# Optimization experiments

Measured on AMD Instinct MI355X. Metric: run time of the kernel, lower is better.

The kernel has to match this reference:

```python
import jax, jax.numpy as jnp
import numpy as np

N, E, DIN, H, M, O = 100000, 3200000, 128, 256, 500, 100


def setup_inputs() -> dict:
    key = jax.random.key(0)
    ks = jax.random.split(key, 8)
    x = jax.random.normal(ks[0], (N, DIN), dtype=jnp.float32)
    edge_index = jax.random.randint(ks[1], (2, E), 0, N, dtype=jnp.int64)
    # GCNConv weights (glorot-ish scale) and biases
    W1 = jax.random.normal(ks[2], (DIN, H), dtype=jnp.float32) / np.sqrt(DIN)
    b1 = jnp.zeros((H,), dtype=jnp.float32)
    W2 = jax.random.normal(ks[3], (H, M), dtype=jnp.float32) / np.sqrt(H)
    b2 = jnp.zeros((M,), dtype=jnp.float32)
    # output head ('GO'): Linear(M -> O)
    Wout = jax.random.normal(ks[4], (M, O), dtype=jnp.float32) / np.sqrt(M)
    bout = jnp.zeros((O,), dtype=jnp.float32)
    # threshold param stored as inv_softplus(1.0) so softplus(threshold)=1.0
    threshold = jnp.float32(np.log(np.expm1(1.0)))
    return {"x": x, "edge_index": edge_index, "W1": W1, "b1": b1,
            "W2": W2, "b2": b2, "Wout": Wout, "bout": bout,
            "threshold": threshold}


def reference(x, edge_index, W1, b1, W2, b2, Wout, bout, threshold):
    src, dst = edge_index[0], edge_index[1]
    n = x.shape[0]
    # GCN sym-normalization with improved=True (self-loop weight 2):
    # deg[i] = 2 + #incoming edges; norm(e) = deg^-1/2[src] * deg^-1/2[dst]
    deg = jax.ops.segment_sum(jnp.ones(src.shape[0], x.dtype), dst,
                              num_segments=n) + jnp.asarray(2.0, x.dtype)
    dinv = jax.lax.rsqrt(deg)
    coef = dinv[src] * dinv[dst]              # [E]
    self_coef = (2.0 * dinv * dinv)[:, None]  # [N,1] self-loop term

    def gcn_conv(h, W, b):
        h = h @ W                              # [N,C]
        agg = jax.ops.segment_sum(h[src] * coef[:, None], dst, num_segments=n)
        return agg + self_coef * h + b

    h = jax.nn.relu(gcn_conv(x, W1, b1))       # conv + ReLU (no bn, no dropout)
    module_representation = jax.nn.softplus(gcn_conv(h, W2, b2))  # [N,M]
    # tanh probability transform: tanh(softplus(threshold) * x)
    p = jnp.tanh(jax.nn.softplus(threshold) * module_representation)
    y_go = p @ Wout + bout                     # output head 'GO'
    return (module_representation, y_go)
```

## Files before the change

### kernel.cpp

```cpp
#include <hip/hip_runtime.h>
#include <cstdint>
#include <cstddef>

#define DIN 128
#define HID 256
#define MODD 500
#define OUTD 100

typedef unsigned int uint;
typedef unsigned short ushort;
typedef __attribute__((ext_vector_type(8))) __bf16 bf16x8;
typedef __attribute__((ext_vector_type(4))) float f32x4;

__device__ __forceinline__ float bf2f(ushort u) {
    return __uint_as_float(((uint)u) << 16);
}
__device__ __forceinline__ ushort f2bf(float f) {
    uint u = __float_as_uint(f);
    return (ushort)((u + 0x7FFF + ((u >> 16) & 1)) >> 16);
}
__device__ __forceinline__ uint packbf2(float lo, float hi) {
    return (uint)f2bf(lo) | ((uint)f2bf(hi) << 16);
}
__device__ __forceinline__ void async_copy16(const void* g, void* l) {
    __builtin_amdgcn_global_load_lds((const __attribute__((address_space(1))) void*)g,
                                     (__attribute__((address_space(3))) void*)l, 16, 0, 0);
}
__device__ __forceinline__ float tanh_fast(float x) {
    return 1.0f - 2.0f / (__expf(2.0f * x) + 1.0f);
}
__device__ __forceinline__ float softplus_fast(float v) {
    return fmaxf(v, 0.0f) + __logf(1.0f + __expf(-fabsf(v)));
}
__device__ __forceinline__ void acc8(float* a, uint4 v, float w) {
    a[0] += w * bf2f((ushort)(v.x & 0xFFFF));
    a[1] += w * bf2f((ushort)(v.x >> 16));
    a[2] += w * bf2f((ushort)(v.y & 0xFFFF));
    a[3] += w * bf2f((ushort)(v.y >> 16));
    a[4] += w * bf2f((ushort)(v.z & 0xFFFF));
    a[5] += w * bf2f((ushort)(v.z >> 16));
    a[6] += w * bf2f((ushort)(v.w & 0xFFFF));
    a[7] += w * bf2f((ushort)(v.w >> 16));
}


__global__ void count_deg(const int* __restrict__ dst, int* __restrict__ deg, int E) {
    int e = blockIdx.x * blockDim.x + threadIdx.x;
    if (e < E) atomicAdd(&deg[dst[e]], 1);
}

__global__ void compute_dinv(const int* __restrict__ deg, float* __restrict__ dinv, int N) {
    int i = blockIdx.x * blockDim.x + threadIdx.x;
    if (i < N) dinv[i] = rsqrtf((float)deg[i] + 2.0f);
}

__global__ void scan_block(const int* __restrict__ deg, int* __restrict__ rp,
                           int* __restrict__ bsum, int n) {
    __shared__ int wsum[16];
    int tid = threadIdx.x;
    int lane = tid & 63;
    int w = tid >> 6;
    int i = blockIdx.x * 1024 + tid;
    int v = (i < n) ? deg[i] : 0;
    int x = v;
    #pragma unroll
    for (int off = 1; off < 64; off <<= 1) {
        int t = __shfl_up(x, off);
        if (lane >= off) x += t;
    }
    if (lane == 63) wsum[w] = x;
    __syncthreads();
    if (tid == 0) {
        int s = 0;
        #pragma unroll
        for (int k = 0; k < 16; ++k) { int t = wsum[k]; wsum[k] = s; s += t; }
        bsum[blockIdx.x] = s;
    }
    __syncthreads();
    if (i < n) rp[i] = wsum[w] + (x - v);
}

__global__ void scan_bsums(int* __restrict__ bsum, int nb) {
    if (threadIdx.x == 0 && blockIdx.x == 0) {
        int s = 0;
        for (int k = 0; k < nb; ++k) { int t = bsum[k]; bsum[k] = s; s += t; }
        bsum[nb] = s;
    }
}

__global__ void scan_add(int* __restrict__ rp, const int* __restrict__ bsum, int n, int nb) {
    int i = blockIdx.x * blockDim.x + threadIdx.x;
    if (i < n) rp[i] += bsum[i >> 10];
    else if (i == n) rp[n] = bsum[nb];
}


#define BSH 9
#define MAXB 256
#define PCH 8192

__global__ void init_bucket_cursor(const int* __restrict__ rp, int* __restrict__ bcur,
                                   int NB) {
    int b = blockIdx.x * blockDim.x + threadIdx.x;
    if (b < NB) bcur[b] = rp[b << BSH];
}

__global__ __launch_bounds__(256)
void partition_edges(const int* __restrict__ src, const int* __restrict__ dst,
                     int* __restrict__ bcur, uint* __restrict__ pairBuf,
                     int E, int NB) {
    __shared__ int hist[MAXB];
    __shared__ int gbase[MAXB];
    int tid = threadIdx.x;
    int e0 = blockIdx.x * PCH;
    int e1 = min(e0 + PCH, E);
    for (int b = tid; b < NB; b += 256) hist[b] = 0;
    __syncthreads();
    for (int e = e0 + tid; e < e1; e += 256) {
        int d = dst[e];
        atomicAdd(&hist[d >> BSH], 1);
    }
    __syncthreads();
    for (int b = tid; b < NB; b += 256) {
        int h = hist[b];
        gbase[b] = h ? atomicAdd(&bcur[b], h) : 0;
        hist[b] = 0;
    }
    __syncthreads();
    for (int e = e0 + tid; e < e1; e += 256) {
        int d = dst[e];
        int s = src[e];
        int b = d >> BSH;
        int idx = gbase[b] + atomicAdd(&hist[b], 1);
        pairBuf[idx] = (uint)s | ((uint)(d & ((1 << BSH) - 1)) << 20);
    }
}

__global__ __launch_bounds__(512)
void bucket_scatter(const uint* __restrict__ pairBuf, const int* __restrict__ rp,
                    int* __restrict__ col, int N) {
    __shared__ int lcur[1 << BSH];
    int b = blockIdx.x;
    int n0 = b << BSH;
    int nn = min(1 << BSH, N - n0);
    int tid = threadIdx.x;
    for (int i = tid; i < nn; i += 512) lcur[i] = rp[n0 + i];
    __syncthreads();
    int start = rp[n0];
    int end = rp[min(n0 + (1 << BSH), N)];
    for (int e = start + tid; e < end; e += 512) {
        uint v = pairBuf[e];
        int doff = v >> 20;
        int s = v & 0xFFFFF;
        int pos = atomicAdd(&lcur[doff], 1);
        col[pos] = s;
    }
}


__global__ void cast_f32_bf16(const float* __restrict__ src, ushort* __restrict__ dst, int n4) {
    int i = blockIdx.x * blockDim.x + threadIdx.x;
    if (i < n4) {
        float4 v = ((const float4*)src)[i];
        ushort4 o;
        o.x = f2bf(v.x); o.y = f2bf(v.y); o.z = f2bf(v.z); o.w = f2bf(v.w);
        ((ushort4*)dst)[i] = o;
    }
}

__global__ void transpose_cast(const float* __restrict__ src, ushort* __restrict__ dst,
                               int K, int N, int Kpad, int Npad) {
    int idx = blockIdx.x * blockDim.x + threadIdx.x;
    if (idx >= Npad * Kpad) return;
    int n = idx / Kpad, k = idx - n * Kpad;
    float v = (n < N && k < K) ? src[(size_t)k * N + n] : 0.0f;
    dst[idx] = f2bf(v);
}


__global__ void aggregate128(const ushort* __restrict__ X, ushort* __restrict__ Y,
                             const int* __restrict__ rp, const int* __restrict__ col,
                             const float* __restrict__ dinv, int N) {
    int gw = blockIdx.x * (blockDim.x >> 6) + (threadIdx.x >> 6);
    int lane = threadIdx.x & 63;
    if (gw >= N) return;
    int g = lane >> 4;
    int sub = lane & 15;
    float di = dinv[gw];
    float sc = 2.0f * di * di;
    const uint4* Xr = (const uint4*)X;
    float a[8] = {};
    if (g == 0) acc8(a, Xr[(size_t)gw * 16 + sub], sc);
    int e = rp[gw], end = rp[gw + 1];
    int base = e;
    for (; base + 8 <= end; base += 8) {
        int c0 = col[base + g];
        int c1 = col[base + 4 + g];
        float w0 = dinv[c0] * di, w1 = dinv[c1] * di;
        uint4 v0 = Xr[(size_t)c0 * 16 + sub];
        uint4 v1 = Xr[(size_t)c1 * 16 + sub];
        acc8(a, v0, w0);
        acc8(a, v1, w1);
    }
    if (base + 4 <= end) {
        int c0 = col[base + g];
        float w0 = dinv[c0] * di;
        acc8(a, Xr[(size_t)c0 * 16 + sub], w0);
        base += 4;
    }
    int rem = end - base;
    if (g < rem) {
        int c0 = col[base + g];
        float w0 = dinv[c0] * di;
        acc8(a, Xr[(size_t)c0 * 16 + sub], w0);
    }
    #pragma unroll
    for (int q = 0; q < 8; ++q) {
        a[q] += __shfl_xor(a[q], 16);
        a[q] += __shfl_xor(a[q], 32);
    }
    if (g == 0) {
        uint4 o;
        o.x = packbf2(a[0], a[1]);
        o.y = packbf2(a[2], a[3]);
        o.z = packbf2(a[4], a[5]);
        o.w = packbf2(a[6], a[7]);
        ((uint4*)Y)[(size_t)gw * 16 + sub] = o;
    }
}

__global__ void aggregate256(const ushort* __restrict__ X, ushort* __restrict__ Y,
                             const int* __restrict__ rp, const int* __restrict__ col,
                             const float* __restrict__ dinv, int N) {
    int gw = blockIdx.x * (blockDim.x >> 6) + (threadIdx.x >> 6);
    int lane = threadIdx.x & 63;
    if (gw >= N) return;
    int g = lane >> 5;
    int sub = lane & 31;
    float di = dinv[gw];
    float sc = 2.0f * di * di;
    const uint4* Xr = (const uint4*)X;
    float a[8] = {};
    if (g == 0) acc8(a, Xr[(size_t)gw * 32 + sub], sc);
    int e = rp[gw], end = rp[gw + 1];
    int base = e;
    for (; base + 4 <= end; base += 4) {
        int c0 = col[base + g];
        int c1 = col[base + 2 + g];
        float w0 = dinv[c0] * di, w1 = dinv[c1] * di;
        uint4 v0 = Xr[(size_t)c0 * 32 + sub];
        uint4 v1 = Xr[(size_t)c1 * 32 + sub];
        acc8(a, v0, w0);
        acc8(a, v1, w1);
    }
    if (base + 2 <= end) {
        int c0 = col[base + g];
        float w0 = dinv[c0] * di;
        acc8(a, Xr[(size_t)c0 * 32 + sub], w0);
        base += 2;
    }
    if (base < end && g == 0) {
        int c0 = col[base];
        float w0 = dinv[c0] * di;
        acc8(a, Xr[(size_t)c0 * 32 + sub], w0);
    }
    #pragma unroll
    for (int q = 0; q < 8; ++q) a[q] += __shfl_xor(a[q], 32);
    if (g == 0) {
        uint4 o;
        o.x = packbf2(a[0], a[1]);
        o.y = packbf2(a[2], a[3]);
        o.z = packbf2(a[4], a[5]);
        o.w = packbf2(a[6], a[7]);
        ((uint4*)Y)[(size_t)gw * 32 + sub] = o;
    }
}


template<int K, int MODE>
__global__ __launch_bounds__(256)
void gemm_bt(const ushort* __restrict__ A, const ushort* __restrict__ BT,
             const float* __restrict__ bias, void* __restrict__ Cout,
             int M, int Nact, int ldc, ushort* __restrict__ C2,
             const float* __restrict__ thr) {
    __shared__ ushort sA[128 * 32];
    __shared__ ushort sB[128 * 32];
    int tid = threadIdx.x;
    int lane = tid & 63;
    int w = tid >> 6;
    int wr = w >> 1, wc = w & 1;
    int row0 = blockIdx.y * 128;
    int col0 = blockIdx.x * 128;
    float sp = 0.0f;
    if (MODE == 3) sp = softplus_fast(*thr);
    f32x4 acc[4][4] = {};

    for (int kt = 0; kt < K; kt += 32) {
        if (kt) __syncthreads();
        #pragma unroll
        for (int L = 0; L < 2; ++L) {
            int cb = L * 256 + w * 64;
            int c = cb + lane;
            int r = c >> 2;
            int ko = (c & 3) * 8;
            int rr = min(row0 + r, M - 1);
            async_copy16(A + (size_t)rr * K + kt + ko, sA + (size_t)cb * 8);
        }
        #pragma unroll
        for (int L = 0; L < 2; ++L) {
            int cb = L * 256 + w * 64;
            int c = cb + lane;
            int nr = c >> 2;
            int ko = (c & 3) * 8;
            async_copy16(BT + (size_t)(col0 + nr) * K + kt + ko, sB + (size_t)cb * 8);
        }
        __syncthreads();
        bf16x8 af[4], bfr[4];
        #pragma unroll
        for (int i = 0; i < 4; ++i) {
            int row = wr * 64 + i * 16 + (lane & 15);
            af[i] = *(const bf16x8*)(sA + row * 32 + (lane >> 4) * 8);
        }
        #pragma unroll
        for (int j = 0; j < 4; ++j) {
            int n = wc * 64 + j * 16 + (lane & 15);
            bfr[j] = *(const bf16x8*)(sB + n * 32 + (lane >> 4) * 8);
        }
        #pragma unroll
        for (int i = 0; i < 4; ++i)
            #pragma unroll
            for (int j = 0; j < 4; ++j)
                acc[i][j] = __builtin_amdgcn_mfma_f32_16x16x32_bf16(af[i], bfr[j], acc[i][j], 0, 0, 0);
    }

    #pragma unroll
    for (int i = 0; i < 4; ++i) {
        #pragma unroll
        for (int j = 0; j < 4; ++j) {
            int col = col0 + wc * 64 + j * 16 + (lane & 15);
            if (MODE == 3) {
                bool act = (col < Nact);
                float bv = act ? bias[col] : 0.0f;
                #pragma unroll
                for (int r = 0; r < 4; ++r) {
                    int row = row0 + wr * 64 + i * 16 + (lane >> 4) * 4 + r;
                    if (row >= M) continue;
                    if (act) {
                        float v = softplus_fast(acc[i][j][r] + bv);
                        ((float*)Cout)[(size_t)row * ldc + col] = v;
                        C2[(size_t)row * 512 + col] = f2bf(tanh_fast(sp * v));
                    } else {
                        C2[(size_t)row * 512 + col] = 0;
                    }
                }
            } else {
                if (col >= Nact) continue;
                float bv = bias[col];
                #pragma unroll
                for (int r = 0; r < 4; ++r) {
                    int row = row0 + wr * 64 + i * 16 + (lane >> 4) * 4 + r;
                    if (row >= M) continue;
                    float v = acc[i][j][r] + bv;
                    if (MODE == 0) {
                        v = fmaxf(v, 0.0f);
                        ((ushort*)Cout)[(size_t)row * ldc + col] = f2bf(v);
                    } else {
                        ((float*)Cout)[(size_t)row * ldc + col] = v;
                    }
                }
            }
        }
    }
}


extern "C" void kernel_launch(void* const* d_in, const int* in_sizes, int n_in,
                              void* d_out, int out_size, void* d_ws, size_t ws_size,
                              hipStream_t stream) {
    const float* x    = (const float*)d_in[0];
    const int*   ei   = (const int*)d_in[1];
    const float* W1   = (const float*)d_in[2];
    const float* b1   = (const float*)d_in[3];
    const float* W2   = (const float*)d_in[4];
    const float* b2   = (const float*)d_in[5];
    const float* Wout = (const float*)d_in[6];
    const float* bout = (const float*)d_in[7];
    const float* thr  = (const float*)d_in[8];

    int N = in_sizes[0] / DIN;
    int E = in_sizes[1] / 2;
    const int* srcI = ei;
    const int* dstI = ei + E;

    char* wsp = (char*)d_ws;
    size_t o = 0;
    auto alloc = [&](size_t bytes) -> void* {
        void* p = wsp + o;
        o = (o + bytes + 255) & ~(size_t)255;
        return p;
    };
    int*    deg   = (int*)alloc((size_t)N * 4);
    float*  dinv  = (float*)alloc((size_t)N * 4);
    int*    rp    = (int*)alloc((size_t)(N + 1) * 4);
    int*    bsum  = (int*)alloc(1024);
    int*    bcur  = (int*)alloc(MAXB * 4);
    ushort* W1T   = (ushort*)alloc((size_t)256 * 128 * 2);
    ushort* W2T   = (ushort*)alloc((size_t)512 * 256 * 2);
    ushort* WoutT = (ushort*)alloc((size_t)128 * 512 * 2);
    ushort* bufA  = (ushort*)alloc((size_t)N * 256 * 2);
    size_t  col_off = o;
    int*    col   = (int*)alloc((size_t)E * 4);
    ushort* hbuf  = (ushort*)alloc((size_t)N * 256 * 2);
    size_t  pbf_need = col_off + (size_t)N * 512 * 2;
    if (o < pbf_need) o = (pbf_need + 255) & ~(size_t)255;
    ushort* pbf = (ushort*)(wsp + col_off);

    ushort* xbf = bufA;
    ushort* xa  = bufA + (size_t)N * 128;
    ushort* ha  = bufA;
    uint* pairBuf = (uint*)hbuf;

    float* mr   = (float*)d_out;
    float* yout = (float*)d_out + (size_t)N * MODD;

    int mtiles = (N + 127) / 128;
    int NB = (N + (1 << BSH) - 1) >> BSH;

    hipMemsetAsync(deg, 0, (size_t)N * 4, stream);
    count_deg<<<(E + 255) / 256, 256, 0, stream>>>(dstI, deg, E);
    compute_dinv<<<(N + 255) / 256, 256, 0, stream>>>(deg, dinv, N);
    int nb = (N + 1023) / 1024;
    scan_block<<<nb, 1024, 0, stream>>>(deg, rp, bsum, N);
    scan_bsums<<<1, 64, 0, stream>>>(bsum, nb);
    scan_add<<<(N + 256) / 256, 256, 0, stream>>>(rp, bsum, N, nb);
    init_bucket_cursor<<<1, 256, 0, stream>>>(rp, bcur, NB);
    partition_edges<<<(E + PCH - 1) / PCH, 256, 0, stream>>>(srcI, dstI, bcur, pairBuf, E, NB);
    bucket_scatter<<<NB, 512, 0, stream>>>(pairBuf, rp, col, N);

    cast_f32_bf16<<<((N * DIN / 4) + 255) / 256, 256, 0, stream>>>(x, xbf, N * DIN / 4);
    transpose_cast<<<(256 * 128 + 255) / 256, 256, 0, stream>>>(W1, W1T, 128, 256, 128, 256);
    transpose_cast<<<(512 * 256 + 255) / 256, 256, 0, stream>>>(W2, W2T, 256, 500, 256, 512);
    transpose_cast<<<(128 * 512 + 255) / 256, 256, 0, stream>>>(Wout, WoutT, 500, 100, 512, 128);

    aggregate128<<<(N + 3) / 4, 256, 0, stream>>>(xbf, xa, rp, col, dinv, N);
    gemm_bt<128, 0><<<dim3(2, mtiles), 256, 0, stream>>>(xa, W1T, b1, hbuf, N, HID, HID,
                                                         nullptr, nullptr);

    aggregate256<<<(N + 3) / 4, 256, 0, stream>>>(hbuf, ha, rp, col, dinv, N);
    gemm_bt<256, 3><<<dim3(4, mtiles), 256, 0, stream>>>(ha, W2T, b2, mr, N, MODD, MODD,
                                                         pbf, thr);

    gemm_bt<512, 2><<<dim3(1, mtiles), 256, 0, stream>>>(pbf, WoutT, bout, yout, N, OUTD, OUTD,
                                                         nullptr, nullptr);
}
```

Measured before the change: 1.072 ms.

## Sort edges by source bin within each bucket and use nontemporal output stores

Inside each destination bucket, bucket_scatter now histograms edges by source-node bin, prefix-sums the counts and reorders the packed pairs into a scratch buffer before scattering them into the CSR column array. Edges within each row therefore come out roughly ordered by source, which is meant to improve locality of the feature gathers in the later aggregation kernels. The fp32 output stores in the GEMM epilogues also switch to nontemporal stores to reduce cache pollution from the large output writes. The cost is an extra pass over pairBuf plus scratch traffic, and the scratch buffer aliases bufA, which is only safe because bufA is written later.

```diff
diff --git a/kernel.cpp b/kernel.cpp
--- a/kernel.cpp
+++ b/kernel.cpp
@@ -138,18 +138,55 @@
 
 __global__ __launch_bounds__(512)
 void bucket_scatter(const uint* __restrict__ pairBuf, const int* __restrict__ rp,
-                    int* __restrict__ col, int N) {
+                    int* __restrict__ col, uint* __restrict__ scratch, int N) {
     __shared__ int lcur[1 << BSH];
+    __shared__ int hist[MAXB];
+    __shared__ int bincur[MAXB];
+    __shared__ int wsum2[4];
+    int tid = threadIdx.x;
+    int lane = tid & 63;
+    int w = tid >> 6;
     int b = blockIdx.x;
     int n0 = b << BSH;
     int nn = min(1 << BSH, N - n0);
-    int tid = threadIdx.x;
-    for (int i = tid; i < nn; i += 512) lcur[i] = rp[n0 + i];
-    __syncthreads();
     int start = rp[n0];
     int end = rp[min(n0 + (1 << BSH), N)];
+
+    for (int i = tid; i < MAXB; i += 512) hist[i] = 0;
+    __syncthreads();
+    for (int e = start + tid; e < end; e += 512)
+        atomicAdd(&hist[(pairBuf[e] & 0xFFFFF) >> BSH], 1);
+    __syncthreads();
+    int xv = 0, vv = 0;
+    if (tid < 256) {
+        vv = hist[tid];
+        xv = vv;
+        #pragma unroll
+        for (int off = 1; off < 64; off <<= 1) {
+            int t = __shfl_up(xv, off);
+            if (lane >= off) xv += t;
+        }
+        if (lane == 63) wsum2[w] = xv;
+    }
+    __syncthreads();
+    if (tid == 0) {
+        int s = 0;
+        #pragma unroll
+        for (int k = 0; k < 4; ++k) { int t = wsum2[k]; wsum2[k] = s; s += t; }
+    }
+    __syncthreads();
+    if (tid < 256) bincur[tid] = wsum2[w] + (xv - vv);
+    __syncthreads();
     for (int e = start + tid; e < end; e += 512) {
         uint v = pairBuf[e];
+        int bin = (v & 0xFFFFF) >> BSH;
+        int p = start + atomicAdd(&bincur[bin], 1);
+        scratch[p] = v;
+    }
+    for (int i = tid; i < nn; i += 512) lcur[i] = rp[n0 + i];
+    __syncthreads();
+    for (int e = start + tid; e < end; e += 512) {
+        uint v = scratch[e];
         int doff = v >> 20;
         int s = v & 0xFFFFF;
         int pos = atomicAdd(&lcur[doff], 1);
@@ -347,7 +384,7 @@
                     if (row >= M) continue;
                     if (act) {
                         float v = softplus_fast(acc[i][j][r] + bv);
-                        ((float*)Cout)[(size_t)row * ldc + col] = v;
+                        __builtin_nontemporal_store(v, &((float*)Cout)[(size_t)row * ldc + col]);
                         C2[(size_t)row * 512 + col] = f2bf(tanh_fast(sp * v));
                     } else {
                         C2[(size_t)row * 512 + col] = 0;
@@ -365,7 +402,7 @@
                         v = fmaxf(v, 0.0f);
                         ((ushort*)Cout)[(size_t)row * ldc + col] = f2bf(v);
                     } else {
-                        ((float*)Cout)[(size_t)row * ldc + col] = v;
+                        __builtin_nontemporal_store(v, &((float*)Cout)[(size_t)row * ldc + col]);
                     }
                 }
             }
@@ -419,6 +456,7 @@
     ushort* xa  = bufA + (size_t)N * 128;
     ushort* ha  = bufA;
     uint* pairBuf = (uint*)hbuf;
+    uint* scratch = (uint*)bufA;
 
     float* mr   = (float*)d_out;
     float* yout = (float*)d_out + (size_t)N * MODD;
@@ -435,7 +473,7 @@
     scan_add<<<(N + 256) / 256, 256, 0, stream>>>(rp, bsum, N, nb);
     init_bucket_cursor<<<1, 256, 0, stream>>>(rp, bcur, NB);
     partition_edges<<<(E + PCH - 1) / PCH, 256, 0, stream>>>(srcI, dstI, bcur, pairBuf, E, NB);
-    bucket_scatter<<<NB, 512, 0, stream>>>(pairBuf, rp, col, N);
+    bucket_scatter<<<NB, 512, 0, stream>>>(pairBuf, rp, col, scratch, N);
 
     cast_f32_bf16<<<((N * DIN / 4) + 255) / 256, 256, 0, stream>>>(x, xbf, N * DIN / 4);
     transpose_cast<<<(256 * 128 + 255) / 256, 256, 0, stream>>>(W1, W1T, 128, 256, 128, 256);
```

After: 1.181 ms. 1.1x slower.

## Build CSR from bucket counts, computing per-node degree and dinv inside bucket scatter

Applied to the files above, without the earlier changes.

Replaces the global per-node atomic degree count and the multi-kernel prefix scan with a per-bucket histogram (shared-memory atomics), a tiny single-thread bucket scan, and a per-bucket local count and scan inside bucket_scatter, which then writes row pointers and dinv. This removes 3.2M global atomics on scattered addresses and several launches. In exchange, bucket_scatter reads pairBuf twice and the bucket count pass reads dst an extra time.

```diff
diff --git a/kernel.cpp b/kernel.cpp
--- a/kernel.cpp
+++ b/kernel.cpp
@@ -44,65 +44,34 @@
 }
 
 
-__global__ void count_deg(const int* __restrict__ dst, int* __restrict__ deg, int E) {
-    int e = blockIdx.x * blockDim.x + threadIdx.x;
-    if (e < E) atomicAdd(&deg[dst[e]], 1);
-}
-
-__global__ void compute_dinv(const int* __restrict__ deg, float* __restrict__ dinv, int N) {
-    int i = blockIdx.x * blockDim.x + threadIdx.x;
-    if (i < N) dinv[i] = rsqrtf((float)deg[i] + 2.0f);
-}
-
-__global__ void scan_block(const int* __restrict__ deg, int* __restrict__ rp,
-                           int* __restrict__ bsum, int n) {
-    __shared__ int wsum[16];
-    int tid = threadIdx.x;
-    int lane = tid & 63;
-    int w = tid >> 6;
-    int i = blockIdx.x * 1024 + tid;
-    int v = (i < n) ? deg[i] : 0;
-    int x = v;
-    #pragma unroll
-    for (int off = 1; off < 64; off <<= 1) {
-        int t = __shfl_up(x, off);
-        if (lane >= off) x += t;
-    }
-    if (lane == 63) wsum[w] = x;
-    __syncthreads();
-    if (tid == 0) {
-        int s = 0;
-        #pragma unroll
-        for (int k = 0; k < 16; ++k) { int t = wsum[k]; wsum[k] = s; s += t; }
-        bsum[blockIdx.x] = s;
-    }
-    __syncthreads();
-    if (i < n) rp[i] = wsum[w] + (x - v);
-}
-
-__global__ void scan_bsums(int* __restrict__ bsum, int nb) {
-    if (threadIdx.x == 0 && blockIdx.x == 0) {
-        int s = 0;
-        for (int k = 0; k < nb; ++k) { int t = bsum[k]; bsum[k] = s; s += t; }
-        bsum[nb] = s;
-    }
-}
-
-__global__ void scan_add(int* __restrict__ rp, const int* __restrict__ bsum, int n, int nb) {
-    int i = blockIdx.x * blockDim.x + threadIdx.x;
-    if (i < n) rp[i] += bsum[i >> 10];
-    else if (i == n) rp[n] = bsum[nb];
-}
-
-
 #define BSH 9
 #define MAXB 256
 #define PCH 8192
 
-__global__ void init_bucket_cursor(const int* __restrict__ rp, int* __restrict__ bcur,
-                                   int NB) {
-    int b = blockIdx.x * blockDim.x + threadIdx.x;
-    if (b < NB) bcur[b] = rp[b << BSH];
+__global__ __launch_bounds__(256)
+void bucket_count(const int* __restrict__ dst, int* __restrict__ btot, int E, int NB) {
+    __shared__ int hist[MAXB];
+    int tid = threadIdx.x;
+    int e0 = blockIdx.x * PCH;
+    int e1 = min(e0 + PCH, E);
+    for (int b = tid; b < MAXB; b += 256) hist[b] = 0;
+    __syncthreads();
+    for (int e = e0 + tid; e < e1; e += 256)
+        atomicAdd(&hist[dst[e] >> BSH], 1);
+    __syncthreads();
+    for (int b = tid; b < NB; b += 256)
+        if (hist[b]) atomicAdd(&btot[b], hist[b]);
+}
+
+__global__ void scan_buckets(const int* __restrict__ btot, int* __restrict__ bstart,
+                             int* __restrict__ bcur, int* __restrict__ rp,
+                             int NB, int N, int E) {
+    if (threadIdx.x == 0 && blockIdx.x == 0) {
+        int s = 0;
+        for (int b = 0; b < NB; ++b) { bstart[b] = s; bcur[b] = s; s += btot[b]; }
+        bstart[NB] = s;
+        rp[N] = E;
+    }
 }
 
 __global__ __launch_bounds__(256)
@@ -137,23 +106,52 @@
 }
 
 __global__ __launch_bounds__(512)
-void bucket_scatter(const uint* __restrict__ pairBuf, const int* __restrict__ rp,
-                    int* __restrict__ col, int N) {
+void bucket_scatter(const uint* __restrict__ pairBuf, const int* __restrict__ bstart,
+                    int* __restrict__ col, int* __restrict__ rp,
+                    float* __restrict__ dinv, int N) {
+    __shared__ int lcnt[1 << BSH];
     __shared__ int lcur[1 << BSH];
+    __shared__ int wsum[8];
+    int tid = threadIdx.x;
+    int lane = tid & 63;
+    int w = tid >> 6;
     int b = blockIdx.x;
     int n0 = b << BSH;
     int nn = min(1 << BSH, N - n0);
-    int tid = threadIdx.x;
-    for (int i = tid; i < nn; i += 512) lcur[i] = rp[n0 + i];
-    __syncthreads();
-    int start = rp[n0];
-    int end = rp[min(n0 + (1 << BSH), N)];
+    int start = bstart[b];
+    int end = bstart[b + 1];
+
+    lcnt[tid] = 0;
+    __syncthreads();
+    for (int e = start + tid; e < end; e += 512)
+        atomicAdd(&lcnt[pairBuf[e] >> 20], 1);
+    __syncthreads();
+    int cnt = lcnt[tid];
+    int x = cnt;
+    #pragma unroll
+    for (int off = 1; off < 64; off <<= 1) {
+        int t = __shfl_up(x, off);
+        if (lane >= off) x += t;
+    }
+    if (lane == 63) wsum[w] = x;
+    __syncthreads();
+    if (tid == 0) {
+        int s = 0;
+        #pragma unroll
+        for (int k = 0; k < 8; ++k) { int t = wsum[k]; wsum[k] = s; s += t; }
+    }
+    __syncthreads();
+    int excl = start + wsum[w] + (x - cnt);
+    if (tid < nn) {
+        rp[n0 + tid] = excl;
+        dinv[n0 + tid] = rsqrtf((float)cnt + 2.0f);
+    }
+    lcur[tid] = excl;
+    __syncthreads();
     for (int e = start + tid; e < end; e += 512) {
         uint v = pairBuf[e];
-        int doff = v >> 20;
-        int s = v & 0xFFFFF;
-        int pos = atomicAdd(&lcur[doff], 1);
-        col[pos] = s;
+        int pos = atomicAdd(&lcur[v >> 20], 1);
+        col[pos] = (int)(v & 0xFFFFF);
     }
 }
 
@@ -399,15 +397,15 @@
         o = (o + bytes + 255) & ~(size_t)255;
         return p;
     };
-    int*    deg   = (int*)alloc((size_t)N * 4);
-    float*  dinv  = (float*)alloc((size_t)N * 4);
-    int*    rp    = (int*)alloc((size_t)(N + 1) * 4);
-    int*    bsum  = (int*)alloc(1024);
-    int*    bcur  = (int*)alloc(MAXB * 4);
-    ushort* W1T   = (ushort*)alloc((size_t)256 * 128 * 2);
-    ushort* W2T   = (ushort*)alloc((size_t)512 * 256 * 2);
-    ushort* WoutT = (ushort*)alloc((size_t)128 * 512 * 2);
-    ushort* bufA  = (ushort*)alloc((size_t)N * 256 * 2);
+    float*  dinv   = (float*)alloc((size_t)N * 4);
+    int*    rp     = (int*)alloc((size_t)(N + 1) * 4);
+    int*    btot   = (int*)alloc(MAXB * 4);
+    int*    bstart = (int*)alloc((MAXB + 1) * 4);
+    int*    bcur   = (int*)alloc(MAXB * 4);
+    ushort* W1T    = (ushort*)alloc((size_t)256 * 128 * 2);
+    ushort* W2T    = (ushort*)alloc((size_t)512 * 256 * 2);
+    ushort* WoutT  = (ushort*)alloc((size_t)128 * 512 * 2);
+    ushort* bufA   = (ushort*)alloc((size_t)N * 256 * 2);
     size_t  col_off = o;
     int*    col   = (int*)alloc((size_t)E * 4);
     ushort* hbuf  = (ushort*)alloc((size_t)N * 256 * 2);
@@ -426,16 +424,11 @@
     int mtiles = (N + 127) / 128;
     int NB = (N + (1 << BSH) - 1) >> BSH;
 
-    hipMemsetAsync(deg, 0, (size_t)N * 4, stream);
-    count_deg<<<(E + 255) / 256, 256, 0, stream>>>(dstI, deg, E);
-    compute_dinv<<<(N + 255) / 256, 256, 0, stream>>>(deg, dinv, N);
-    int nb = (N + 1023) / 1024;
-    scan_block<<<nb, 1024, 0, stream>>>(deg, rp, bsum, N);
-    scan_bsums<<<1, 64, 0, stream>>>(bsum, nb);
-    scan_add<<<(N + 256) / 256, 256, 0, stream>>>(rp, bsum, N, nb);
-    init_bucket_cursor<<<1, 256, 0, stream>>>(rp, bcur, NB);
+    hipMemsetAsync(btot, 0, (size_t)NB * 4, stream);
+    bucket_count<<<(E + PCH - 1) / PCH, 256, 0, stream>>>(dstI, btot, E, NB);
+    scan_buckets<<<1, 64, 0, stream>>>(btot, bstart, bcur, rp, NB, N, E);
     partition_edges<<<(E + PCH - 1) / PCH, 256, 0, stream>>>(srcI, dstI, bcur, pairBuf, E, NB);
-    bucket_scatter<<<NB, 512, 0, stream>>>(pairBuf, rp, col, N);
+    bucket_scatter<<<NB, 512, 0, stream>>>(pairBuf, bstart, col, rp, dinv, N);
 
     cast_f32_bf16<<<((N * DIN / 4) + 255) / 256, 256, 0, stream>>>(x, xbf, N * DIN / 4);
     transpose_cast<<<(256 * 128 + 255) / 256, 256, 0, stream>>>(W1, W1T, 128, 256, 128, 256);
```

New measurement: 959.3 us. 10.5% less time.
